# Performance work log

Measured on AMD Instinct MI355X. Metric: run time of the kernel, lower is better.

## Reference

```python
import jax, jax.numpy as jnp
import numpy as np

DIM = 1024
NUM_HEADS = 16
HEAD_DIM = DIM // NUM_HEADS


def setup_inputs() -> dict:
    key = jax.random.key(0)
    k1, k2, k3, k4, k5, k6 = jax.random.split(key, 6)
    B, T, C = 4, 2048, DIM
    s = 1.0 / np.sqrt(C)
    return {
        "x": jax.random.normal(k1, (B, T, C), dtype=jnp.float32),
        "attn_bias": jax.random.normal(k2, (B, T, T), dtype=jnp.float32),
        "qkv_w": jax.random.uniform(k3, (3 * C, C), dtype=jnp.float32, minval=-s, maxval=s),
        "qkv_b": jax.random.uniform(k4, (3 * C,), dtype=jnp.float32, minval=-s, maxval=s),
        "out_w": jax.random.uniform(k5, (C, C), dtype=jnp.float32, minval=-s, maxval=s),
        "out_b": jax.random.uniform(k6, (C,), dtype=jnp.float32, minval=-s, maxval=s),
    }


def reference(x, attn_bias, qkv_w, qkv_b, out_w, out_b):
    B, T, C = x.shape
    H, D = NUM_HEADS, HEAD_DIM
    # fused QKV projection (torch Linear: x @ W^T + b)
    qkv = jnp.einsum('btc,fc->btf', x, qkv_w) + qkv_b  # [B,T,3C]
    q, k, v = jnp.split(qkv, 3, axis=-1)
    q = q.reshape(B, T, H, D).transpose(0, 2, 1, 3)  # [B,H,T,D]
    k = k.reshape(B, T, H, D).transpose(0, 2, 1, 3)
    v = v.reshape(B, T, H, D).transpose(0, 2, 1, 3)
    scores = jnp.einsum('bhtd,bhsd->bhts', q, k) / jnp.sqrt(jnp.float32(D))
    scores = scores + attn_bias[:, None, :, :]  # 3-D bias -> broadcast over heads
    attn = jax.nn.softmax(scores, axis=-1)
    out = jnp.einsum('bhts,bhsd->bhtd', attn, v)  # [B,H,T,D]
    out = out.transpose(0, 2, 1, 3).reshape(B, T, C)
    return jnp.einsum('btc,fc->btf', out, out_w) + out_b
```

## Files before the change

### kernel.cpp

```cpp
#include <hip/hip_runtime.h>

#define BATCH 4
#define SEQ   2048
#define CDIM  1024
#define HEADS 16
#define HDIM  64
#define N3    3072
#define NTOK  8192
#define QKP   2048
#define LOG2E 1.44269504f
#define QSC   0.18033688f

typedef __attribute__((ext_vector_type(4))) float    float4v;
typedef __attribute__((ext_vector_type(8))) short    short8;
typedef __attribute__((ext_vector_type(8))) __bf16   bf16x8;
typedef __attribute__((ext_vector_type(4))) _Float16 half4v;
typedef __attribute__((ext_vector_type(2))) _Float16 half2v;

__device__ __forceinline__ unsigned short f2bf(float f) {
    union { float f; unsigned int u; } x; x.f = f;
    unsigned int r = x.u + 0x7fffu + ((x.u >> 16) & 1u);
    return (unsigned short)(r >> 16);
}

__device__ __forceinline__ bf16x8 ld_bf8(const unsigned short* p) {
    short8 s = *(const short8*)p;
    return __builtin_bit_cast(bf16x8, s);
}

__device__ __forceinline__ void glds16(const void* g, void* l) {
    __builtin_amdgcn_global_load_lds(
        (const __attribute__((address_space(1))) void*)g,
        (__attribute__((address_space(3))) void*)l, 16, 0, 0);
}

__global__ void cast_f32_bf16(const float* __restrict__ in,
                              unsigned short* __restrict__ out, int n4) {
    int i = blockIdx.x * blockDim.x + threadIdx.x;
    if (i >= n4) return;
    float4v v = ((const float4v*)in)[i];
    ushort4 r;
    r.x = f2bf(v[0]); r.y = f2bf(v[1]); r.z = f2bf(v[2]); r.w = f2bf(v[3]);
    ((ushort4*)out)[i] = r;
}

__global__ __launch_bounds__(256, 3)
void gemm_bt(const unsigned short* __restrict__ A,
             const unsigned short* __restrict__ Bm,
             const float* __restrict__ bias,
             void* __restrict__ Cout,
             void* __restrict__ Cout2,
             int M, int N, int K, int mode)
{
    __shared__ alignas(16) unsigned short As[128 * 64];
    __shared__ alignas(16) unsigned short Bs[128 * 64];

    const int tid  = threadIdx.x;
    const int lane = tid & 63;
    const int wave = tid >> 6;
    const int wr = wave >> 1, wc = wave & 1;
    const int lm = lane & 15, quad = lane >> 4;
    const size_t m0 = (size_t)blockIdx.y * 128;
    const size_t n0 = (size_t)blockIdx.x * 128;

    const unsigned short* ag[4];
    const unsigned short* bg[4];
    unsigned short* la[4];
    unsigned short* lb[4];
#pragma unroll
    for (int i = 0; i < 4; i++) {
        int idx = tid + i * 256;
        int row = idx >> 3;
        int lc  = (idx & 7) ^ (row & 7);
        ag[i] = &A [(m0 + row) * K + lc * 8];
        bg[i] = &Bm[(n0 + row) * K + lc * 8];
        la[i] = &As[(idx & ~63) * 8];
        lb[i] = &Bs[(idx & ~63) * 8];
    }

    float4v acc[4][4];
#pragma unroll
    for (int i = 0; i < 4; i++)
#pragma unroll
        for (int j = 0; j < 4; j++) acc[i][j] = (float4v){0.f, 0.f, 0.f, 0.f};

    for (int k0 = 0; k0 < K; k0 += 64) {
#pragma unroll
        for (int i = 0; i < 4; i++) glds16(ag[i], la[i]);
#pragma unroll
        for (int i = 0; i < 4; i++) glds16(bg[i], lb[i]);
#pragma unroll
        for (int i = 0; i < 4; i++) { ag[i] += 64; bg[i] += 64; }
        __syncthreads();
#pragma unroll
        for (int kk = 0; kk < 2; kk++) {
            bf16x8 af[4], bfr[4];
#pragma unroll
            for (int t = 0; t < 4; t++) {
                int slot = ((quad + kk * 4) ^ (lm & 7)) * 8;
                af [t] = ld_bf8(&As[(wr * 64 + t * 16 + lm) * 64 + slot]);
                bfr[t] = ld_bf8(&Bs[(wc * 64 + t * 16 + lm) * 64 + slot]);
            }
#pragma unroll
            for (int ti = 0; ti < 4; ti++)
#pragma unroll
                for (int tj = 0; tj < 4; tj++)
                    acc[ti][tj] = __builtin_amdgcn_mfma_f32_16x16x32_bf16(
                        af[ti], bfr[tj], acc[ti][tj], 0, 0, 0);
        }
        __syncthreads();
    }

#pragma unroll
    for (int ti = 0; ti < 4; ti++) {
        size_t row = m0 + wr * 64 + ti * 16 + quad * 4;
#pragma unroll
        for (int tj = 0; tj < 4; tj++) {
            int col = (int)n0 + wc * 64 + tj * 16 + lm;
            float bv = bias[col];
            if (mode == 0) {
#pragma unroll
                for (int r = 0; r < 4; r++)
                    ((float*)Cout)[(row + r) * N + col] = acc[ti][tj][r] + bv;
            } else if (col < 2 * CDIM) {
                float scl = (col < CDIM) ? QSC : 1.0f;
#pragma unroll
                for (int r = 0; r < 4; r++)
                    ((unsigned short*)Cout)[(row + r) * QKP + col] =
                        f2bf((acc[ti][tj][r] + bv) * scl);
            } else {
                int hd = col - 2 * CDIM;
                int bb = (int)(row >> 11);
                int s  = (int)(row & 2047);
                half4v hv;
#pragma unroll
                for (int r = 0; r < 4; r++) hv[r] = (_Float16)(acc[ti][tj][r] + bv);
                *(half4v*)((unsigned short*)Cout2 +
                           ((size_t)bb * CDIM + hd) * SEQ + s) = hv;
            }
        }
    }
}

__global__ __launch_bounds__(256, 4)
void attn_kernel(const unsigned short* __restrict__ qk,
                 const unsigned short* __restrict__ vT,
                 const float* __restrict__ bias,
                 unsigned short* __restrict__ outp)
{
    __shared__ alignas(16) char smem[32768];
    float*          BiasS = (float*)smem;
    unsigned short* Qs    = (unsigned short*)smem;
    unsigned short* Ks    = (unsigned short*)(smem + 16384);
    unsigned short* Vts   = (unsigned short*)(smem + 24576);

    const int tid  = threadIdx.x;
    const int lane = tid & 63, wave = tid >> 6;
    const int lm = lane & 15, quad = lane >> 4;
    const int q0 = blockIdx.x * 64;
    const int bh = blockIdx.y;
    const int bb = bh >> 4, h = bh & 15;
    const size_t rowbase = (size_t)bb * SEQ;
    const unsigned short* vTh = vT + (size_t)bh * HDIM * SEQ;
    const float* biasb = bias + (size_t)bb * SEQ * SEQ + (size_t)q0 * SEQ;

#pragma unroll
    for (int i = 0; i < 2; i++) {
        int idx = tid + i * 256;
        int row = idx >> 3;
        int lc  = (idx & 7) ^ (row & 7);
        glds16(&qk[(rowbase + q0 + row) * QKP + h * 64 + lc * 8], &Qs[(idx & ~63) * 8]);
    }
    __syncthreads();
    bf16x8 bq[2];
#pragma unroll
    for (int kk = 0; kk < 2; kk++)
        bq[kk] = ld_bf8(&Qs[(wave * 16 + lm) * 64 + (((quad + kk * 4) ^ (lm & 7)) * 8)]);

    const unsigned short *kg0, *kg1, *vg0, *vg1;
    unsigned short *lk0, *lk1, *lv0, *lv1;
    {
        int idx = tid, row = idx >> 3, lc = (idx & 7) ^ (row & 7);
        kg0 = &qk[(rowbase + row) * QKP + CDIM + h * 64 + lc * 8];
        vg0 = &vTh[(size_t)row * SEQ + lc * 8];
        lk0 = &Ks[(idx & ~63) * 8];
        lv0 = &Vts[(idx & ~63) * 8];
        idx = tid + 256; row = idx >> 3; lc = (idx & 7) ^ (row & 7);
        kg1 = &qk[(rowbase + row) * QKP + CDIM + h * 64 + lc * 8];
        vg1 = &vTh[(size_t)row * SEQ + lc * 8];
        lk1 = &Ks[(idx & ~63) * 8];
        lv1 = &Vts[(idx & ~63) * 8];
    }
    const float* bgp[4];
    float*       lbp[4];
#pragma unroll
    for (int i = 0; i < 4; i++) {
        int idx = tid + i * 256;
        int row = idx >> 4;
        int lc  = (idx & 15) ^ (row & 15);
        bgp[i] = &biasb[(size_t)row * SEQ + lc * 4];
        lbp[i] = &BiasS[(idx & ~63) * 4];
    }

    const half4v vones = {(_Float16)1.f, (_Float16)1.f, (_Float16)1.f, (_Float16)1.f};
    float4v rs4 = (float4v){0.f, 0.f, 0.f, 0.f};
    float4v o[4];
#pragma unroll
    for (int t = 0; t < 4; t++) o[t] = (float4v){0.f, 0.f, 0.f, 0.f};

    for (int it = 0; it < SEQ / 64; ++it) {
        __syncthreads();
        glds16(kg0, lk0); glds16(kg1, lk1);
        glds16(vg0, lv0); glds16(vg1, lv1);
#pragma unroll
        for (int i = 0; i < 4; i++) glds16(bgp[i], lbp[i]);
        kg0 += 64 * QKP; kg1 += 64 * QKP;
        vg0 += 64; vg1 += 64;
#pragma unroll
        for (int i = 0; i < 4; i++) bgp[i] += 64;
        __syncthreads();

        float4v st[4];
#pragma unroll
        for (int tj = 0; tj < 4; tj++) {
            float4v bv = *(const float4v*)&BiasS[(wave * 16 + lm) * 64 +
                                                 (((tj * 4 + quad) ^ lm) * 4)];
            st[tj] = bv * LOG2E;
            bf16x8 ak0 = ld_bf8(&Ks[(tj * 16 + lm) * 64 + (((quad    ) ^ (lm & 7)) * 8)]);
            bf16x8 ak1 = ld_bf8(&Ks[(tj * 16 + lm) * 64 + (((quad + 4) ^ (lm & 7)) * 8)]);
            st[tj] = __builtin_amdgcn_mfma_f32_16x16x32_bf16(ak0, bq[0], st[tj], 0, 0, 0);
            st[tj] = __builtin_amdgcn_mfma_f32_16x16x32_bf16(ak1, bq[1], st[tj], 0, 0, 0);
        }

        half4v pa[4];
#pragma unroll
        for (int tj = 0; tj < 4; tj++) {
            float p0 = __builtin_amdgcn_exp2f(st[tj][0]);
            float p1 = __builtin_amdgcn_exp2f(st[tj][1]);
            float p2 = __builtin_amdgcn_exp2f(st[tj][2]);
            float p3 = __builtin_amdgcn_exp2f(st[tj][3]);
            half2v plo = __builtin_bit_cast(half2v, __builtin_amdgcn_cvt_pkrtz(p0, p1));
            half2v phi = __builtin_bit_cast(half2v, __builtin_amdgcn_cvt_pkrtz(p2, p3));
            pa[tj][0] = plo[0]; pa[tj][1] = plo[1];
            pa[tj][2] = phi[0]; pa[tj][3] = phi[1];
        }

#pragma unroll
        for (int tj = 0; tj < 4; tj++)
            rs4 = __builtin_amdgcn_mfma_f32_16x16x16f16(pa[tj], vones, rs4, 0, 0, 0);

#pragma unroll
        for (int tj = 0; tj < 4; tj++) {
            int c = tj * 4 + quad;
#pragma unroll
            for (int dt = 0; dt < 4; dt++) {
                int row = dt * 16 + lm;
                int off = (((c >> 1) ^ (lm & 7)) * 8) + (c & 1) * 4;
                half4v vb = *(const half4v*)&Vts[row * 64 + off];
                o[dt] = __builtin_amdgcn_mfma_f32_16x16x16f16(pa[tj], vb, o[dt], 0, 0, 0);
            }
        }
    }

    float i4[4];
#pragma unroll
    for (int r = 0; r < 4; r++) i4[r] = 1.0f / rs4[r];
#pragma unroll
    for (int dt = 0; dt < 4; dt++) {
        int col = h * 64 + dt * 16 + lm;
#pragma unroll
        for (int r = 0; r < 4; r++) {
            size_t trow = rowbase + q0 + wave * 16 + quad * 4 + r;
            outp[trow * CDIM + col] = f2bf(o[dt][r] * i4[r]);
        }
    }
}

extern "C" void kernel_launch(void* const* d_in, const int* in_sizes, int n_in,
                              void* d_out, int out_size, void* d_ws, size_t ws_size,
                              hipStream_t stream)
{
    const float* x         = (const float*)d_in[0];
    const float* attn_bias = (const float*)d_in[1];
    const float* qkv_w     = (const float*)d_in[2];
    const float* qkv_b     = (const float*)d_in[3];
    const float* out_w     = (const float*)d_in[4];
    const float* out_b     = (const float*)d_in[5];
    float* out = (float*)d_out;

    char* p = (char*)d_ws;
    unsigned short* x_bf   = (unsigned short*)p; p += (size_t)NTOK * CDIM * 2;
    unsigned short* wq_bf  = (unsigned short*)p; p += (size_t)N3 * CDIM * 2;
    unsigned short* wo_bf  = (unsigned short*)p; p += (size_t)CDIM * CDIM * 2;
    unsigned short* qk_bf  = (unsigned short*)p; p += (size_t)NTOK * QKP * 2;
    unsigned short* vT_f16 = (unsigned short*)p; p += (size_t)BATCH * CDIM * SEQ * 2;
    unsigned short* at_bf  = (unsigned short*)p;

    int n4;
    n4 = NTOK * CDIM / 4;
    cast_f32_bf16<<<(n4 + 255) / 256, 256, 0, stream>>>(x, x_bf, n4);
    n4 = N3 * CDIM / 4;
    cast_f32_bf16<<<(n4 + 255) / 256, 256, 0, stream>>>(qkv_w, wq_bf, n4);
    n4 = CDIM * CDIM / 4;
    cast_f32_bf16<<<(n4 + 255) / 256, 256, 0, stream>>>(out_w, wo_bf, n4);

    gemm_bt<<<dim3(N3 / 128, NTOK / 128), 256, 0, stream>>>(
        x_bf, wq_bf, qkv_b, qk_bf, vT_f16, NTOK, N3, CDIM, 1);

    attn_kernel<<<dim3(SEQ / 64, BATCH * HEADS), 256, 0, stream>>>(
        qk_bf, vT_f16, attn_bias, at_bf);

    gemm_bt<<<dim3(CDIM / 128, NTOK / 128), 256, 0, stream>>>(
        at_bf, wo_bf, out_b, out, nullptr, NTOK, CDIM, CDIM, 0);
}
```

Measured before the change: 353.2 us.

## Double-buffer K/V tiles and load bias directly to registers in attention

Replaces the single-buffered shared-memory K/V/bias tiles with double-buffered K and V tiles, issuing the next tile's async loads before computing the current one, so one barrier per step replaces two. The attention bias is now read straight from global memory into registers, prefetched one step ahead, instead of being staged through LDS. Q is loaded directly from global memory into registers. The MFMA section is wrapped in s_setprio. The last iteration redundantly prefetches tile 0 through the wraparound index, and the register prefetch of bias raises register pressure.

```diff
diff --git a/kernel.cpp b/kernel.cpp
--- a/kernel.cpp
+++ b/kernel.cpp
@@ -148,11 +148,8 @@
                  const float* __restrict__ bias,
                  unsigned short* __restrict__ outp)
 {
-    __shared__ alignas(16) char smem[32768];
-    float*          BiasS = (float*)smem;
-    unsigned short* Qs    = (unsigned short*)smem;
-    unsigned short* Ks    = (unsigned short*)(smem + 16384);
-    unsigned short* Vts   = (unsigned short*)(smem + 24576);
+    __shared__ alignas(16) unsigned short Ks[2][64 * 64];
+    __shared__ alignas(16) unsigned short Vts[2][64 * 64];
 
     const int tid  = threadIdx.x;
     const int lane = tid & 63, wave = tid >> 6;
@@ -164,43 +161,27 @@
     const unsigned short* vTh = vT + (size_t)bh * HDIM * SEQ;
     const float* biasb = bias + (size_t)bb * SEQ * SEQ + (size_t)q0 * SEQ;
 
-#pragma unroll
-    for (int i = 0; i < 2; i++) {
-        int idx = tid + i * 256;
-        int row = idx >> 3;
-        int lc  = (idx & 7) ^ (row & 7);
-        glds16(&qk[(rowbase + q0 + row) * QKP + h * 64 + lc * 8], &Qs[(idx & ~63) * 8]);
-    }
-    __syncthreads();
     bf16x8 bq[2];
-#pragma unroll
-    for (int kk = 0; kk < 2; kk++)
-        bq[kk] = ld_bf8(&Qs[(wave * 16 + lm) * 64 + (((quad + kk * 4) ^ (lm & 7)) * 8)]);
-
-    const unsigned short *kg0, *kg1, *vg0, *vg1;
-    unsigned short *lk0, *lk1, *lv0, *lv1;
+    {
+        const unsigned short* qrow =
+            &qk[(rowbase + q0 + wave * 16 + lm) * QKP + h * 64];
+        bq[0] = ld_bf8(qrow + (quad    ) * 8);
+        bq[1] = ld_bf8(qrow + (quad + 4) * 8);
+    }
+
+    const unsigned short *kgb0, *kgb1, *vgb0, *vgb1;
+    int ldo0, ldo1;
     {
         int idx = tid, row = idx >> 3, lc = (idx & 7) ^ (row & 7);
-        kg0 = &qk[(rowbase + row) * QKP + CDIM + h * 64 + lc * 8];
-        vg0 = &vTh[(size_t)row * SEQ + lc * 8];
-        lk0 = &Ks[(idx & ~63) * 8];
-        lv0 = &Vts[(idx & ~63) * 8];
+        kgb0 = &qk[(rowbase + row) * QKP + CDIM + h * 64 + lc * 8];
+        vgb0 = &vTh[(size_t)row * SEQ + lc * 8];
+        ldo0 = (idx & ~63) * 8;
         idx = tid + 256; row = idx >> 3; lc = (idx & 7) ^ (row & 7);
-        kg1 = &qk[(rowbase + row) * QKP + CDIM + h * 64 + lc * 8];
-        vg1 = &vTh[(size_t)row * SEQ + lc * 8];
-        lk1 = &Ks[(idx & ~63) * 8];
-        lv1 = &Vts[(idx & ~63) * 8];
-    }
-    const float* bgp[4];
-    float*       lbp[4];
-#pragma unroll
-    for (int i = 0; i < 4; i++) {
-        int idx = tid + i * 256;
-        int row = idx >> 4;
-        int lc  = (idx & 15) ^ (row & 15);
-        bgp[i] = &biasb[(size_t)row * SEQ + lc * 4];
-        lbp[i] = &BiasS[(idx & ~63) * 4];
-    }
+        kgb1 = &qk[(rowbase + row) * QKP + CDIM + h * 64 + lc * 8];
+        vgb1 = &vTh[(size_t)row * SEQ + lc * 8];
+        ldo1 = (idx & ~63) * 8;
+    }
+    const float* bbase = biasb + (size_t)(wave * 16 + lm) * SEQ + quad * 4;
 
     const half4v vones = {(_Float16)1.f, (_Float16)1.f, (_Float16)1.f, (_Float16)1.f};
     float4v rs4 = (float4v){0.f, 0.f, 0.f, 0.f};
@@ -208,59 +189,77 @@
 #pragma unroll
     for (int t = 0; t < 4; t++) o[t] = (float4v){0.f, 0.f, 0.f, 0.f};
 
-    for (int it = 0; it < SEQ / 64; ++it) {
-        __syncthreads();
-        glds16(kg0, lk0); glds16(kg1, lk1);
-        glds16(vg0, lv0); glds16(vg1, lv1);
-#pragma unroll
-        for (int i = 0; i < 4; i++) glds16(bgp[i], lbp[i]);
-        kg0 += 64 * QKP; kg1 += 64 * QKP;
-        vg0 += 64; vg1 += 64;
-#pragma unroll
-        for (int i = 0; i < 4; i++) bgp[i] += 64;
-        __syncthreads();
-
-        float4v st[4];
-#pragma unroll
-        for (int tj = 0; tj < 4; tj++) {
-            float4v bv = *(const float4v*)&BiasS[(wave * 16 + lm) * 64 +
-                                                 (((tj * 4 + quad) ^ lm) * 4)];
-            st[tj] = bv * LOG2E;
-            bf16x8 ak0 = ld_bf8(&Ks[(tj * 16 + lm) * 64 + (((quad    ) ^ (lm & 7)) * 8)]);
-            bf16x8 ak1 = ld_bf8(&Ks[(tj * 16 + lm) * 64 + (((quad + 4) ^ (lm & 7)) * 8)]);
-            st[tj] = __builtin_amdgcn_mfma_f32_16x16x32_bf16(ak0, bq[0], st[tj], 0, 0, 0);
-            st[tj] = __builtin_amdgcn_mfma_f32_16x16x32_bf16(ak1, bq[1], st[tj], 0, 0, 0);
-        }
-
-        half4v pa[4];
-#pragma unroll
-        for (int tj = 0; tj < 4; tj++) {
-            float p0 = __builtin_amdgcn_exp2f(st[tj][0]);
-            float p1 = __builtin_amdgcn_exp2f(st[tj][1]);
-            float p2 = __builtin_amdgcn_exp2f(st[tj][2]);
-            float p3 = __builtin_amdgcn_exp2f(st[tj][3]);
-            half2v plo = __builtin_bit_cast(half2v, __builtin_amdgcn_cvt_pkrtz(p0, p1));
-            half2v phi = __builtin_bit_cast(half2v, __builtin_amdgcn_cvt_pkrtz(p2, p3));
-            pa[tj][0] = plo[0]; pa[tj][1] = plo[1];
-            pa[tj][2] = phi[0]; pa[tj][3] = phi[1];
-        }
-
-#pragma unroll
-        for (int tj = 0; tj < 4; tj++)
-            rs4 = __builtin_amdgcn_mfma_f32_16x16x16f16(pa[tj], vones, rs4, 0, 0, 0);
-
-#pragma unroll
-        for (int tj = 0; tj < 4; tj++) {
-            int c = tj * 4 + quad;
-#pragma unroll
-            for (int dt = 0; dt < 4; dt++) {
-                int row = dt * 16 + lm;
-                int off = (((c >> 1) ^ (lm & 7)) * 8) + (c & 1) * 4;
-                half4v vb = *(const half4v*)&Vts[row * 64 + off];
-                o[dt] = __builtin_amdgcn_mfma_f32_16x16x16f16(pa[tj], vb, o[dt], 0, 0, 0);
-            }
-        }
-    }
+    float4v bA[4], bB[4];
+
+    glds16(kgb0, &Ks[0][0]  + ldo0);
+    glds16(kgb1, &Ks[0][0]  + ldo1);
+    glds16(vgb0, &Vts[0][0] + ldo0);
+    glds16(vgb1, &Vts[0][0] + ldo1);
+#pragma unroll
+    for (int tj = 0; tj < 4; ++tj)
+        bA[tj] = *(const float4v*)(bbase + tj * 16);
+    __syncthreads();
+
+#define ATTN_STEP(IT, KSC, VSC, KSN, VSN, BC, BN) do {                         \
+    int itn = ((IT) + 1) & 31;                                                 \
+    size_t ko = (size_t)itn * 64 * QKP;                                        \
+    int    vo = itn * 64;                                                      \
+    glds16(kgb0 + ko, (KSN) + ldo0);                                           \
+    glds16(kgb1 + ko, (KSN) + ldo1);                                           \
+    glds16(vgb0 + vo, (VSN) + ldo0);                                           \
+    glds16(vgb1 + vo, (VSN) + ldo1);                                           \
+    _Pragma("unroll")                                                          \
+    for (int tj = 0; tj < 4; ++tj)                                             \
+        (BN)[tj] = *(const float4v*)(bbase + (size_t)itn * 64 + tj * 16);      \
+                                         \
+    float4v st[4];                                                             \
+    _Pragma("unroll")                                                          \
+    for (int tj = 0; tj < 4; ++tj) {                                           \
+        st[tj] = (BC)[tj] * LOG2E;                                             \
+        bf16x8 ak0 = ld_bf8(&(KSC)[(tj * 16 + lm) * 64 + (((quad    ) ^ (lm & 7)) * 8)]); \
+        bf16x8 ak1 = ld_bf8(&(KSC)[(tj * 16 + lm) * 64 + (((quad + 4) ^ (lm & 7)) * 8)]); \
+        st[tj] = __builtin_amdgcn_mfma_f32_16x16x32_bf16(ak0, bq[0], st[tj], 0, 0, 0); \
+        st[tj] = __builtin_amdgcn_mfma_f32_16x16x32_bf16(ak1, bq[1], st[tj], 0, 0, 0); \
+    }                                                                          \
+                                                \
+    half4v pa[4];                                                              \
+    _Pragma("unroll")                                                          \
+    for (int tj = 0; tj < 4; ++tj) {                                           \
+        float p0 = __builtin_amdgcn_exp2f(st[tj][0]);                          \
+        float p1 = __builtin_amdgcn_exp2f(st[tj][1]);                          \
+        float p2 = __builtin_amdgcn_exp2f(st[tj][2]);                          \
+        float p3 = __builtin_amdgcn_exp2f(st[tj][3]);                          \
+        half2v plo = __builtin_bit_cast(half2v, __builtin_amdgcn_cvt_pkrtz(p0, p1)); \
+        half2v phi = __builtin_bit_cast(half2v, __builtin_amdgcn_cvt_pkrtz(p2, p3)); \
+        pa[tj][0] = plo[0]; pa[tj][1] = plo[1];                                \
+        pa[tj][2] = phi[0]; pa[tj][3] = phi[1];                                \
+    }                                                                          \
+                                                     \
+    _Pragma("unroll")                                                          \
+    for (int tj = 0; tj < 4; ++tj)                                             \
+        rs4 = __builtin_amdgcn_mfma_f32_16x16x16f16(pa[tj], vones, rs4, 0, 0, 0); \
+                                                                 \
+    __builtin_amdgcn_s_setprio(1);                                             \
+    _Pragma("unroll")                                                          \
+    for (int tj = 0; tj < 4; ++tj) {                                           \
+        int c = tj * 4 + quad;                                                 \
+        _Pragma("unroll")                                                      \
+        for (int dt = 0; dt < 4; ++dt) {                                       \
+            int row = dt * 16 + lm;                                            \
+            int off = (((c >> 1) ^ (lm & 7)) * 8) + (c & 1) * 4;               \
+            half4v vb = *(const half4v*)&(VSC)[row * 64 + off];                 \
+            o[dt] = __builtin_amdgcn_mfma_f32_16x16x16f16(pa[tj], vb, o[dt], 0, 0, 0); \
+        }                                                                      \
+    }                                                                          \
+    __builtin_amdgcn_s_setprio(0);                                             \
+    __syncthreads();       \
+} while (0)
+
+    for (int itp = 0; itp < 16; ++itp) {
+        ATTN_STEP(2 * itp,     &Ks[0][0], &Vts[0][0], &Ks[1][0], &Vts[1][0], bA, bB);
+        ATTN_STEP(2 * itp + 1, &Ks[1][0], &Vts[1][0], &Ks[0][0], &Vts[0][0], bB, bA);
+    }
+#undef ATTN_STEP
 
     float i4[4];
 #pragma unroll
```

New measurement: 396.2 us. 1.12x slower.

## Enlarge attention query tile to 128 with 512 threads, swizzle GEMM blocks across XCDs

Applied to the files above, without the earlier changes.

The attention kernel now processes 128 query rows per block with 8 waves, so each K/V tile loaded into shared memory is reused by twice as many queries. Q is read straight from global memory into registers instead of being staged through LDS, and the PV MFMA section runs at raised wave priority. The GEMM remaps block indices so consecutive workgroups land on the same XCD's L2. The trade-off is a larger LDS footprint for the bias tile and fewer blocks in the attention grid.

```diff
diff --git a/kernel.cpp b/kernel.cpp
--- a/kernel.cpp
+++ b/kernel.cpp
@@ -60,8 +60,15 @@
     const int wave = tid >> 6;
     const int wr = wave >> 1, wc = wave & 1;
     const int lm = lane & 15, quad = lane >> 4;
-    const size_t m0 = (size_t)blockIdx.y * 128;
-    const size_t n0 = (size_t)blockIdx.x * 128;
+
+    const int nwg  = gridDim.x * gridDim.y;
+    const int d    = blockIdx.y * gridDim.x + blockIdx.x;
+    const int orig = (d & 7) * (nwg >> 3) + (d >> 3);
+    const int bix  = orig % gridDim.x;
+    const int biy  = orig / gridDim.x;
+
+    const size_t m0 = (size_t)biy * 128;
+    const size_t n0 = (size_t)bix * 128;
 
     const unsigned short* ag[4];
     const unsigned short* bg[4];
@@ -142,60 +149,48 @@
     }
 }
 
-__global__ __launch_bounds__(256, 4)
+__global__ __launch_bounds__(512, 6)
 void attn_kernel(const unsigned short* __restrict__ qk,
                  const unsigned short* __restrict__ vT,
                  const float* __restrict__ bias,
                  unsigned short* __restrict__ outp)
 {
-    __shared__ alignas(16) char smem[32768];
-    float*          BiasS = (float*)smem;
-    unsigned short* Qs    = (unsigned short*)smem;
-    unsigned short* Ks    = (unsigned short*)(smem + 16384);
-    unsigned short* Vts   = (unsigned short*)(smem + 24576);
+    __shared__ alignas(16) unsigned short Ks [64 * 64];
+    __shared__ alignas(16) unsigned short Vts[64 * 64];
+    __shared__ alignas(16) float          BiasS[128 * 64];
 
     const int tid  = threadIdx.x;
     const int lane = tid & 63, wave = tid >> 6;
     const int lm = lane & 15, quad = lane >> 4;
-    const int q0 = blockIdx.x * 64;
+    const int q0 = blockIdx.x * 128;
     const int bh = blockIdx.y;
     const int bb = bh >> 4, h = bh & 15;
     const size_t rowbase = (size_t)bb * SEQ;
     const unsigned short* vTh = vT + (size_t)bh * HDIM * SEQ;
     const float* biasb = bias + (size_t)bb * SEQ * SEQ + (size_t)q0 * SEQ;
 
-#pragma unroll
-    for (int i = 0; i < 2; i++) {
-        int idx = tid + i * 256;
-        int row = idx >> 3;
-        int lc  = (idx & 7) ^ (row & 7);
-        glds16(&qk[(rowbase + q0 + row) * QKP + h * 64 + lc * 8], &Qs[(idx & ~63) * 8]);
-    }
-    __syncthreads();
     bf16x8 bq[2];
-#pragma unroll
-    for (int kk = 0; kk < 2; kk++)
-        bq[kk] = ld_bf8(&Qs[(wave * 16 + lm) * 64 + (((quad + kk * 4) ^ (lm & 7)) * 8)]);
-
-    const unsigned short *kg0, *kg1, *vg0, *vg1;
-    unsigned short *lk0, *lk1, *lv0, *lv1;
+    {
+        const unsigned short* qrow =
+            &qk[(rowbase + q0 + wave * 16 + lm) * QKP + h * 64];
+        bq[0] = ld_bf8(qrow + (quad    ) * 8);
+        bq[1] = ld_bf8(qrow + (quad + 4) * 8);
+    }
+
+    const unsigned short *kg0, *vg0;
+    unsigned short *lk0, *lv0;
     {
         int idx = tid, row = idx >> 3, lc = (idx & 7) ^ (row & 7);
         kg0 = &qk[(rowbase + row) * QKP + CDIM + h * 64 + lc * 8];
         vg0 = &vTh[(size_t)row * SEQ + lc * 8];
-        lk0 = &Ks[(idx & ~63) * 8];
+        lk0 = &Ks [(idx & ~63) * 8];
         lv0 = &Vts[(idx & ~63) * 8];
-        idx = tid + 256; row = idx >> 3; lc = (idx & 7) ^ (row & 7);
-        kg1 = &qk[(rowbase + row) * QKP + CDIM + h * 64 + lc * 8];
-        vg1 = &vTh[(size_t)row * SEQ + lc * 8];
-        lk1 = &Ks[(idx & ~63) * 8];
-        lv1 = &Vts[(idx & ~63) * 8];
     }
     const float* bgp[4];
     float*       lbp[4];
 #pragma unroll
     for (int i = 0; i < 4; i++) {
-        int idx = tid + i * 256;
+        int idx = tid + i * 512;
         int row = idx >> 4;
         int lc  = (idx & 15) ^ (row & 15);
         bgp[i] = &biasb[(size_t)row * SEQ + lc * 4];
@@ -210,19 +205,19 @@
 
     for (int it = 0; it < SEQ / 64; ++it) {
         __syncthreads();
-        glds16(kg0, lk0); glds16(kg1, lk1);
-        glds16(vg0, lv0); glds16(vg1, lv1);
+        glds16(kg0, lk0);
+        glds16(vg0, lv0);
 #pragma unroll
         for (int i = 0; i < 4; i++) glds16(bgp[i], lbp[i]);
-        kg0 += 64 * QKP; kg1 += 64 * QKP;
-        vg0 += 64; vg1 += 64;
+        kg0 += 64 * QKP;
+        vg0 += 64;
 #pragma unroll
         for (int i = 0; i < 4; i++) bgp[i] += 64;
         __syncthreads();
 
         float4v st[4];
 #pragma unroll
-        for (int tj = 0; tj < 4; tj++) {
+        for (int tj = 0; tj < 4; ++tj) {
             float4v bv = *(const float4v*)&BiasS[(wave * 16 + lm) * 64 +
                                                  (((tj * 4 + quad) ^ lm) * 4)];
             st[tj] = bv * LOG2E;
@@ -234,7 +229,7 @@
 
         half4v pa[4];
 #pragma unroll
-        for (int tj = 0; tj < 4; tj++) {
+        for (int tj = 0; tj < 4; ++tj) {
             float p0 = __builtin_amdgcn_exp2f(st[tj][0]);
             float p1 = __builtin_amdgcn_exp2f(st[tj][1]);
             float p2 = __builtin_amdgcn_exp2f(st[tj][2]);
@@ -246,20 +241,22 @@
         }
 
 #pragma unroll
-        for (int tj = 0; tj < 4; tj++)
+        for (int tj = 0; tj < 4; ++tj)
             rs4 = __builtin_amdgcn_mfma_f32_16x16x16f16(pa[tj], vones, rs4, 0, 0, 0);
 
-#pragma unroll
-        for (int tj = 0; tj < 4; tj++) {
+        __builtin_amdgcn_s_setprio(1);
+#pragma unroll
+        for (int tj = 0; tj < 4; ++tj) {
             int c = tj * 4 + quad;
 #pragma unroll
-            for (int dt = 0; dt < 4; dt++) {
+            for (int dt = 0; dt < 4; ++dt) {
                 int row = dt * 16 + lm;
                 int off = (((c >> 1) ^ (lm & 7)) * 8) + (c & 1) * 4;
                 half4v vb = *(const half4v*)&Vts[row * 64 + off];
                 o[dt] = __builtin_amdgcn_mfma_f32_16x16x16f16(pa[tj], vb, o[dt], 0, 0, 0);
             }
         }
+        __builtin_amdgcn_s_setprio(0);
     }
 
     float i4[4];
@@ -307,7 +304,7 @@
     gemm_bt<<<dim3(N3 / 128, NTOK / 128), 256, 0, stream>>>(
         x_bf, wq_bf, qkv_b, qk_bf, vT_f16, NTOK, N3, CDIM, 1);
 
-    attn_kernel<<<dim3(SEQ / 64, BATCH * HEADS), 256, 0, stream>>>(
+    attn_kernel<<<dim3(SEQ / 128, BATCH * HEADS), 512, 0, stream>>>(
         qk_bf, vT_f16, attn_bias, at_bf);
 
     gemm_bt<<<dim3(CDIM / 128, NTOK / 128), 256, 0, stream>>>(
```

After: 374.1 us. +5.9%, slower.
